# Optimization experiments

Measured on AMD Instinct MI355X. Metric: run time of the kernel, lower is better.

Reference implementation:

```python
import jax, jax.numpy as jnp
import numpy as np

LAMBDA_COORD = 5.0
LAMBDA_NOOBJ = 0.5
B, N, F = 2048, 64, 19  # batch, nb_pred, 2 + n_classes


def _greedy_scan(Permut, v, h, D2, mask, n):
    # One greedy-assignment phase: n sequential argmax/one-hot steps.
    def step(carry, _):
        Permut, v, h, D2 = carry
        D2 = D2 * v[:, :, None] * h[:, None, :]
        A = jax.nn.one_hot(jnp.argmax(D2, axis=-1), n, dtype=D2.dtype)          # row-wise best col
        Bm = v[:, :, None] * A * D2
        C = jnp.swapaxes(jax.nn.one_hot(jnp.argmax(Bm, axis=-2), n, dtype=D2.dtype), -1, -2)  # col-wise best row
        E = v[:, :, None] * A * C
        Permut = Permut + E
        v = (1.0 - Permut.sum(-1)) * mask
        h = 1.0 - Permut.sum(-2)
        return (Permut, v, h, D2), None
    (Permut, v, h, D2), _ = jax.lax.scan(step, (Permut, v, h, D2), None, length=n)
    return Permut, v, h, D2


def _permute_ypred(y_true, y_pred):
    alpha = y_true[:, :, 0]                      # [B, N] in {0,1}
    x = y_true[:, :, 1]
    p = y_pred[:, :, 1]
    n = x.shape[-1]
    D1 = 1.0 - jnp.abs(x[:, :, None] - p[:, None, :])   # [B, N, N] similarity

    # Phase 1: match ground-truth positives (rows with alpha=1).
    Permut0 = jnp.zeros_like(D1)
    v0 = alpha
    h0 = jnp.ones_like(alpha)
    D2_0 = v0[:, :, None] * D1
    Permut, v, h, _ = _greedy_scan(Permut0, v0, h0, D2_0, alpha, n)

    # Phase 2: match remaining rows (alpha=0) to remaining predictions.
    neg = 1.0 - alpha
    D2_1 = neg[:, :, None] * D1 * h[:, None, :]
    Permut, _, _, _ = _greedy_scan(Permut, neg, h, D2_1, neg, n)

    permutation = jnp.argmax(Permut, axis=-1)            # [B, N]
    idx = jnp.broadcast_to(permutation[:, :, None], y_pred.shape)
    return jnp.take_along_axis(y_pred, idx, axis=1)


def setup_inputs() -> dict:
    key = jax.random.key(0)
    k1, k2, k3 = jax.random.split(key, 3)
    y_true = jax.random.uniform(k1, (B, N, F), dtype=jnp.float32)
    alpha = (jax.random.uniform(k3, (B, N)) < 0.3).astype(jnp.float32)
    y_true = y_true.at[:, :, 0].set(alpha)
    y_pred = jax.random.uniform(k2, (B, N, F), dtype=jnp.float32)
    return {"y_true": y_true, "y_pred": y_pred}


def reference(y_true, y_pred):
    y_pred = _permute_ypred(y_true, y_pred)
    a = y_true[:, :, 0]
    loss = jnp.sum(
        a * LAMBDA_COORD * jnp.square(y_true[:, :, 1] - y_pred[:, :, 1])
        + a * jnp.square(a - y_pred[:, :, 0])
        + (1.0 - a) * LAMBDA_NOOBJ * jnp.square(a - y_pred[:, :, 0])
        + a * jnp.sum(jnp.square(y_true[:, :, 2:] - y_pred[:, :, 2:]), axis=-1)
    )
    return loss
```

## Files before the change

### kernel.cpp

```cpp
#include <hip/hip_runtime.h>
#include <stdint.h>


#define NN 64
#define NF 19
#define ROWF (NN * NF)
#define ROW4 (ROWF / 4)

__device__ __forceinline__ unsigned umin2(unsigned a, unsigned b) {
  return a < b ? a : b;
}

__global__ __launch_bounds__(64, 2) void spotting_loss_kernel(
    const float* __restrict__ yt, const float* __restrict__ yp,
    float* __restrict__ partial)
{
  const int b = blockIdx.x;
  const int i = threadIdx.x;

  __shared__ float yp_sh[ROWF];
  __shared__ unsigned long long key_sh[NN];

  const float* __restrict__ ytb = yt + (size_t)b * ROWF;
  const float4* __restrict__ yp4 = (const float4*)(yp + (size_t)b * ROWF);
  float4* yp_sh4 = (float4*)yp_sh;
#pragma unroll
  for (int t = 0; t < 5; ++t) {
    const int idx = t * NN + i;
    if (idx < ROW4) yp_sh4[idx] = yp4[idx];
  }
  key_sh[i] = 0ull;
  const float alpha = ytb[i * NF + 0];
  const float x     = ytb[i * NF + 1];
  __syncthreads();

  float D1v[NN];
#pragma unroll
  for (int j = 0; j < NN; ++j)
    D1v[j] = 1.0f - fabsf(x - yp_sh[j * NF + 1]);

  unsigned long long hbits = ~0ull;
  int perm = 0, jmax = 0;
  unsigned long long mykey = 0;
  float best = 0.0f;
  unsigned tag = 0;

  for (int phase = 0; phase < 2; ++phase) {
    bool vlive  = (phase == 0) ? (alpha > 0.5f) : (alpha < 0.5f);
    bool rescan = vlive;

    for (int it = 0; it < NN; ++it) {
      if (__ballot(vlive) == 0ull) break;
      ++tag;

      if (rescan) {
        float m[NN];
#pragma unroll
        for (int j = 0; j < NN; ++j)
          m[j] = ((hbits >> j) & 1ull) ? D1v[j] : 0.0f;

        float t32[32], t16[16], t8[8], t4[4];
#pragma unroll
        for (int j = 0; j < 32; ++j) t32[j] = fmaxf(m[j], m[j + 32]);
#pragma unroll
        for (int j = 0; j < 16; ++j) t16[j] = fmaxf(t32[j], t32[j + 16]);
#pragma unroll
        for (int j = 0; j < 8; ++j)  t8[j]  = fmaxf(t16[j], t16[j + 8]);
#pragma unroll
        for (int j = 0; j < 4; ++j)  t4[j]  = fmaxf(t8[j], t8[j + 4]);
        best = fmaxf(fmaxf(t4[0], t4[1]), fmaxf(t4[2], t4[3]));

        unsigned c32[32], c16[16], c8[8], c4[4];
#pragma unroll
        for (int j = 0; j < 32; ++j) {
          const unsigned a0 = (m[j]      == best) ? (unsigned)j        : 255u;
          const unsigned a1 = (m[j + 32] == best) ? (unsigned)(j + 32) : 255u;
          c32[j] = umin2(a0, a1);
        }
#pragma unroll
        for (int j = 0; j < 16; ++j) c16[j] = umin2(c32[j], c32[j + 16]);
#pragma unroll
        for (int j = 0; j < 8; ++j)  c8[j]  = umin2(c16[j], c16[j + 8]);
#pragma unroll
        for (int j = 0; j < 4; ++j)  c4[j]  = umin2(c8[j], c8[j + 4]);
        jmax = (int)umin2(umin2(c4[0], c4[1]), umin2(c4[2], c4[3]));
        rescan = false;
      }

      if (vlive) {
        mykey = ((unsigned long long)tag << 38) |
                ((unsigned long long)__float_as_uint(best) << 6) |
                (unsigned long long)(63 - i);
        atomicMax(&key_sh[jmax], mykey);
      }
      __builtin_amdgcn_wave_barrier();

      const unsigned long long kc = key_sh[i];
      const unsigned long long kw = key_sh[jmax];
      const unsigned long long killed =
          __ballot((unsigned)(kc >> 38) == tag);

      if (vlive) {
        if (kw == mykey) {
          perm = jmax;
          vlive = false;
        } else {
          rescan = true;
        }
      }
      hbits &= ~killed;
      __builtin_amdgcn_wave_barrier();
    }
  }

  const float a = alpha;
  const int pbase = perm * NF;
  const float p0 = yp_sh[pbase + 0];
  const float p1 = yp_sh[pbase + 1];
  const float dx = x - p1;
  const float da = a - p0;
  float s2 = 0.0f;
#pragma unroll
  for (int f = 2; f < NF; ++f) {
    const float d = ytb[i * NF + f] - yp_sh[pbase + f];
    s2 += d * d;
  }
  float l = a * 5.0f * (dx * dx)
          + a * (da * da)
          + (1.0f - a) * 0.5f * (da * da)
          + a * s2;

#pragma unroll
  for (int off = 32; off > 0; off >>= 1) l += __shfl_down(l, off);
  if (i == 0) partial[b] = l;
}

__global__ __launch_bounds__(1024) void reduce_kernel(
    const float* __restrict__ partial, float* __restrict__ out, int n)
{
  __shared__ float wsum[16];
  const int t = threadIdx.x;
  float s = 0.0f;
  for (int idx = t; idx < n; idx += 1024) s += partial[idx];
#pragma unroll
  for (int off = 32; off > 0; off >>= 1) s += __shfl_down(s, off);
  if ((t & 63) == 0) wsum[t >> 6] = s;
  __syncthreads();
  if (t < 64) {
    float v = (t < 16) ? wsum[t] : 0.0f;
#pragma unroll
    for (int off = 32; off > 0; off >>= 1) v += __shfl_down(v, off);
    if (t == 0) out[0] = v;
  }
}

extern "C" void kernel_launch(void* const* d_in, const int* in_sizes, int n_in,
                              void* d_out, int out_size, void* d_ws, size_t ws_size,
                              hipStream_t stream) {
  const float* yt = (const float*)d_in[0];
  const float* yp = (const float*)d_in[1];
  float* out = (float*)d_out;
  float* partial = (float*)d_ws;
  const int B = in_sizes[0] / ROWF;

  spotting_loss_kernel<<<B, 64, 0, stream>>>(yt, yp, partial);
  reduce_kernel<<<1, 1024, 0, stream>>>(partial, out, B);
}
```

Measured before the change: 110.0 us.

## Replace LDS atomic auction with wave-wide shuffle argmax, one match per step

Each iteration now finds the global best (row, column) pair across the wave with a 64-bit shuffle-xor max reduction. It assigns just that one pair, instead of letting every live row bid through LDS atomicMax and resolving many winners per round. This removes the shared-memory key array, the atomics and the wave barriers. A row only rescans when its chosen column is the one taken. The trade-off is up to one iteration per matched row (about 64 in total) instead of a few parallel rounds, with a 6-step 64-bit shuffle reduction on every iteration. Tie-breaking between equal similarities may also differ from the previous parallel scheme.

```diff
diff --git a/kernel.cpp b/kernel.cpp
--- a/kernel.cpp
+++ b/kernel.cpp
@@ -10,6 +10,10 @@
 __device__ __forceinline__ unsigned umin2(unsigned a, unsigned b) {
   return a < b ? a : b;
 }
+__device__ __forceinline__ unsigned long long umax64(unsigned long long a,
+                                                     unsigned long long b) {
+  return a > b ? a : b;
+}
 
 __global__ __launch_bounds__(64, 2) void spotting_loss_kernel(
     const float* __restrict__ yt, const float* __restrict__ yp,
@@ -19,7 +23,6 @@
   const int i = threadIdx.x;
 
   __shared__ float yp_sh[ROWF];
-  __shared__ unsigned long long key_sh[NN];
 
   const float* __restrict__ ytb = yt + (size_t)b * ROWF;
   const float4* __restrict__ yp4 = (const float4*)(yp + (size_t)b * ROWF);
@@ -29,7 +32,6 @@
     const int idx = t * NN + i;
     if (idx < ROW4) yp_sh4[idx] = yp4[idx];
   }
-  key_sh[i] = 0ull;
   const float alpha = ytb[i * NF + 0];
   const float x     = ytb[i * NF + 1];
   __syncthreads();
@@ -41,18 +43,13 @@
 
   unsigned long long hbits = ~0ull;
   int perm = 0, jmax = 0;
-  unsigned long long mykey = 0;
   float best = 0.0f;
-  unsigned tag = 0;
 
   for (int phase = 0; phase < 2; ++phase) {
     bool vlive  = (phase == 0) ? (alpha > 0.5f) : (alpha < 0.5f);
     bool rescan = vlive;
 
-    for (int it = 0; it < NN; ++it) {
-      if (__ballot(vlive) == 0ull) break;
-      ++tag;
-
+    for (int it = 0; it <= NN; ++it) {
       if (rescan) {
         float m[NN];
 #pragma unroll
@@ -87,29 +84,26 @@
         rescan = false;
       }
 
-      if (vlive) {
-        mykey = ((unsigned long long)tag << 38) |
-                ((unsigned long long)__float_as_uint(best) << 6) |
-                (unsigned long long)(63 - i);
-        atomicMax(&key_sh[jmax], mykey);
+      unsigned long long key = vlive
+          ? (((unsigned long long)__float_as_uint(best) << 12) |
+             ((unsigned long long)(63 - i) << 6) |
+             (unsigned long long)(63 - jmax))
+          : 0ull;
+#pragma unroll
+      for (int off = 32; off > 0; off >>= 1)
+        key = umax64(key, (unsigned long long)__shfl_xor(
+                              (unsigned long long)key, off));
+
+      if (key == 0ull) break;
+
+      const int r = 63 - (int)((key >> 6) & 63ull);
+      const int c = 63 - (int)(key & 63ull);
+      if (i == r) {
+        perm = jmax;
+        vlive = false;
       }
-      __builtin_amdgcn_wave_barrier();
-
-      const unsigned long long kc = key_sh[i];
-      const unsigned long long kw = key_sh[jmax];
-      const unsigned long long killed =
-          __ballot((unsigned)(kc >> 38) == tag);
-
-      if (vlive) {
-        if (kw == mykey) {
-          perm = jmax;
-          vlive = false;
-        } else {
-          rescan = true;
-        }
-      }
-      hbits &= ~killed;
-      __builtin_amdgcn_wave_barrier();
+      hbits &= ~(1ull << c);
+      rescan = vlive && (jmax == c);
     }
   }
 
```

Result: slower. 162.4 us (+47.6%).
